# Performance work log

Hardware: AMD Instinct MI355X
Metric: run time of the kernel (lower is better)

The kernel has to match this reference:

```python
import jax, jax.numpy as jnp
import numpy as np

MODEL_DIM = 256
NUM_HEADS = 4
HEAD_DIM = MODEL_DIM // NUM_HEADS
MAX_LEN = 512
EPS = 1e-5


def positional_embedding(n, dim):
    pos = jnp.arange(n, dtype=jnp.float32)[:, None]
    div = jnp.exp(jnp.arange(0, dim, 2, dtype=jnp.float32) * (-np.log(10000.0) / dim))
    pe = jnp.zeros((n, dim), dtype=jnp.float32)
    pe = pe.at[:, 0::2].set(jnp.sin(pos * div))
    pe = pe.at[:, 1::2].set(jnp.cos(pos * div))
    return pe


def layer_norm(x, g, b):
    mu = jnp.mean(x, axis=-1, keepdims=True)
    var = jnp.mean(jnp.square(x - mu), axis=-1, keepdims=True)
    return (x - mu) * jax.lax.rsqrt(var + EPS) * g + b


def setup_inputs() -> dict:
    key = jax.random.key(0)
    ks = jax.random.split(key, 20)
    B, N = 64, 512
    d = MODEL_DIM

    def lin(k, fan_in, fan_out):
        lim = 1.0 / np.sqrt(fan_in)
        return jax.random.uniform(k, (fan_out, fan_in), jnp.float32, -lim, lim)

    def xavier(k, fan_in, fan_out):
        lim = np.sqrt(6.0 / (fan_in + fan_out))
        return jax.random.uniform(k, (fan_out, fan_in), jnp.float32, -lim, lim)

    return {
        "x": jax.random.normal(ks[0], (B, N, 769), jnp.float32),
        "y": jax.random.normal(ks[1], (B, N, 674), jnp.float32),
        "z": jnp.zeros((B, 1), jnp.float32),
        "Wr": lin(ks[2], 769, d), "br": jnp.zeros((d,), jnp.float32),
        "Wf": lin(ks[3], 674, d), "bf": jnp.zeros((d,), jnp.float32),
        "g_x": jnp.ones((d,), jnp.float32), "b_x": jnp.zeros((d,), jnp.float32),
        "g_y": jnp.ones((d,), jnp.float32), "b_y": jnp.zeros((d,), jnp.float32),
        "Wq": xavier(ks[4], d, d), "bq": jnp.zeros((d,), jnp.float32),
        "Wk": xavier(ks[5], d, d), "bk": jnp.zeros((d,), jnp.float32),
        "Wv": xavier(ks[6], d, d), "bv": jnp.zeros((d,), jnp.float32),
        "Wo": xavier(ks[7], d, d), "bo": jnp.zeros((d,), jnp.float32),
        "g_m": jnp.ones((d,), jnp.float32), "b_m": jnp.zeros((d,), jnp.float32),
        "W1": lin(ks[8], d, d), "b1": jnp.zeros((d,), jnp.float32),
        "W2": lin(ks[9], d, d), "b2": jnp.zeros((d,), jnp.float32),
        "Wc": lin(ks[10], d, 2), "bc": jnp.zeros((2,), jnp.float32),
    }


def reference(x, y, z, Wr, br, Wf, bf, g_x, b_x, g_y, b_y,
              Wq, bq, Wk, bk, Wv, bv, Wo, bo, g_m, b_m,
              W1, b1, W2, b2, Wc, bc):
    B, N, _ = x.shape
    d, H, hd = MODEL_DIM, NUM_HEADS, HEAD_DIM
    pe = positional_embedding(MAX_LEN, d)[:N]  # (N, d)

    xp = layer_norm(x @ Wr.T + br + pe[None], g_x, b_x)  # (B,N,d)
    yp = layer_norm(y @ Wf.T + bf + pe[None], g_y, b_y)

    # cross-attention (non-causal, no masks, eval-mode dropout)
    q = (xp @ Wq.T + bq).reshape(B, N, H, hd)
    k = (yp @ Wk.T + bk).reshape(B, N, H, hd)
    v = (yp @ Wv.T + bv).reshape(B, N, H, hd)
    scale = hd ** -0.5
    scores = jnp.einsum("bshd,bthd->bhst", q, k) * scale  # (B,H,N,N)
    attn = jax.nn.softmax(scores, axis=-1)
    ctx = jnp.einsum("bhst,bthd->bshd", attn, v).reshape(B, N, d)
    attn_out = ctx @ Wo.T + bo

    x_res = layer_norm(xp + attn_out, g_m, b_m)
    mlp = jax.nn.relu(x_res @ W1.T + b1) @ W2.T + b2
    x_mlp = x_res + mlp
    pooled = jnp.mean(x_mlp, axis=1)  # (B,d)
    logits = pooled @ Wc.T + bc  # (B,2)
    return logits
```

## Files before the change

### kernel.cpp

```cpp
#include <hip/hip_runtime.h>
#include <hip/hip_bf16.h>

#define B_   64
#define N_   512
#define D_   256
#define H_   4
#define HD_  64

typedef __hip_bfloat16 bf16;
typedef __attribute__((ext_vector_type(8))) short short8;
typedef __attribute__((ext_vector_type(4))) float floatx4;

__device__ __forceinline__ float bf2f(bf16 v) { return __bfloat162float(v); }
__device__ __forceinline__ unsigned short f2us(float f) {
    bf16 h = __float2bfloat16(f);
    union { bf16 h; unsigned short u; } c; c.h = h; return c.u;
}

typedef __attribute__((address_space(1))) const unsigned int asg_u32;
typedef __attribute__((address_space(3))) unsigned int asl_u32;
__device__ __forceinline__ void gl_lds16(const void* g, void* l) {
    __builtin_amdgcn_global_load_lds((asg_u32*)g, (asl_u32*)l, 16, 0, 0);
}

__global__ __launch_bounds__(256)
void convw_k(const float* __restrict__ Wr, const float* __restrict__ Wf,
             const float* __restrict__ Wq, const float* __restrict__ Wk,
             const float* __restrict__ Wv, const float* __restrict__ Wo,
             const float* __restrict__ W1, const float* __restrict__ W2,
             bf16* __restrict__ dst)
{
    const int seg = blockIdx.y;
    const float* src; int Kreal, Kp; size_t off;
    switch (seg) {
        case 0: src = Wr; Kreal = 769; Kp = 800; off = 0; break;
        case 1: src = Wf; Kreal = 674; Kp = 704; off = 256 * 800; break;
        default:
            src = (seg == 2) ? Wq : (seg == 3) ? Wk : (seg == 4) ? Wv
                : (seg == 5) ? Wo : (seg == 6) ? W1 : W2;
            Kreal = 256; Kp = 256;
            off = 256 * 800 + 256 * 704 + (size_t)(seg - 2) * 256 * 256;
            break;
    }
    const int idx = blockIdx.x * 256 + threadIdx.x;
    if (idx >= 256 * Kp / 8) return;
    const int rowk = idx * 8;
    const int n = rowk / Kp, k0 = rowk % Kp;
    unsigned short tmp[8];
    #pragma unroll
    for (int j = 0; j < 8; ++j) {
        int kk = k0 + j;
        tmp[j] = f2us(kk < Kreal ? src[(size_t)n * Kreal + kk] : 0.f);
    }
    *(short8*)&dst[off + (size_t)rowk] = *(short8*)tmp;
}

__global__ __launch_bounds__(256)
void convx_k(const float* __restrict__ src, bf16* __restrict__ dst,
             int Kreal, int Kp)
{
    const int row = blockIdx.x;
    const float* s = src + (size_t)row * Kreal;
    bf16* d = dst + (size_t)row * Kp;
    for (int c = threadIdx.x; c < Kp; c += 256)
        d[c] = __float2bfloat16(c < Kreal ? s[c] : 0.f);
}

__global__ __launch_bounds__(256)
void pe_k(float* __restrict__ pe)
{
    const int n = blockIdx.x, c = threadIdx.x;
    const int j = c & ~1;
    float freq = __expf(-(float)j * (9.210340371976184f / 256.0f));
    float ang = (float)n * freq;
    pe[n * 256 + c] = (c & 1) ? cosf(ang) : sinf(ang);
}

__global__ __launch_bounds__(256)
void gemm_rp(const bf16* __restrict__ A, int lda,
             const bf16* __restrict__ W, int ldw,
             const float* __restrict__ bias, const bf16* __restrict__ res,
             const float* __restrict__ pe,
             const float* __restrict__ g, const float* __restrict__ bln,
             bf16* __restrict__ C, int Kp, int relu)
{
    __shared__ bf16 As[2][4 * 64 * 8];
    __shared__ bf16 Bs[2][4 * 256 * 8];
    __shared__ float s_mu[64][4], s_sq[64][4];

    const int tid = threadIdx.x;
    const int m0 = blockIdx.x * 64;
    const int lane = tid & 63, w = tid >> 6;
    const int fr = lane & 15, quad = lane >> 4;

    const unsigned short* Ap = (const unsigned short*)A + (size_t)(m0 + lane) * lda + w * 8;
    const unsigned short* Wp = (const unsigned short*)W + (size_t)lane * ldw + w * 8;

    floatx4 acc[4][4] = {};

    gl_lds16(Ap, &As[0][(w * 64 + lane) * 8]);
    #pragma unroll
    for (int i = 0; i < 4; ++i)
        gl_lds16(Wp + (size_t)(i * 64) * ldw, &Bs[0][(w * 256 + i * 64 + lane) * 8]);

    int cur = 0;
    for (int k0 = 0; k0 < Kp; k0 += 32) {
        __syncthreads();
        if (k0 + 32 < Kp) {
            const int nb = cur ^ 1;
            gl_lds16(Ap + k0 + 32, &As[nb][(w * 64 + lane) * 8]);
            #pragma unroll
            for (int i = 0; i < 4; ++i)
                gl_lds16(Wp + (size_t)(i * 64) * ldw + k0 + 32,
                         &Bs[nb][(w * 256 + i * 64 + lane) * 8]);
        }
        short8 a[4];
        #pragma unroll
        for (int im = 0; im < 4; ++im)
            a[im] = *(const short8*)&As[cur][(quad * 64 + im * 16 + fr) * 8];
        #pragma unroll
        for (int in = 0; in < 4; ++in) {
            short8 bfrag = *(const short8*)&Bs[cur][(quad * 256 + w * 64 + in * 16 + fr) * 8];
            #pragma unroll
            for (int im = 0; im < 4; ++im)
                acc[im][in] = __builtin_amdgcn_mfma_f32_16x16x32_bf16(
                    a[im], bfrag, acc[im][in], 0, 0, 0);
        }
        cur ^= 1;
    }

    #pragma unroll
    for (int in = 0; in < 4; ++in) {
        const int n = w * 64 + in * 16 + fr;
        const float bi = bias[n];
        #pragma unroll
        for (int im = 0; im < 4; ++im) {
            #pragma unroll
            for (int reg = 0; reg < 4; ++reg) {
                const int m = m0 + im * 16 + quad * 4 + reg;
                float v = acc[im][in][reg] + bi;
                if (pe)   v += pe[((m & (N_ - 1)) << 8) + n];
                if (relu) v = fmaxf(v, 0.f);
                if (res)  v += bf2f(res[((size_t)m << 8) + n]);
                acc[im][in][reg] = v;
            }
        }
    }

    if (g) {
        #pragma unroll
        for (int im = 0; im < 4; ++im) {
            #pragma unroll
            for (int reg = 0; reg < 4; ++reg) {
                float ps = acc[im][0][reg] + acc[im][1][reg]
                         + acc[im][2][reg] + acc[im][3][reg];
                float pq = acc[im][0][reg] * acc[im][0][reg]
                         + acc[im][1][reg] * acc[im][1][reg]
                         + acc[im][2][reg] * acc[im][2][reg]
                         + acc[im][3][reg] * acc[im][3][reg];
                #pragma unroll
                for (int off = 1; off < 16; off <<= 1) {
                    ps += __shfl_xor(ps, off, 64);
                    pq += __shfl_xor(pq, off, 64);
                }
                if (fr == 0) {
                    const int r = im * 16 + quad * 4 + reg;
                    s_mu[r][w] = ps;
                    s_sq[r][w] = pq;
                }
            }
        }
        __syncthreads();
        #pragma unroll
        for (int im = 0; im < 4; ++im) {
            #pragma unroll
            for (int reg = 0; reg < 4; ++reg) {
                const int r = im * 16 + quad * 4 + reg;
                const float mu = (s_mu[r][0] + s_mu[r][1] + s_mu[r][2] + s_mu[r][3])
                                 * (1.f / 256.f);
                const float var = (s_sq[r][0] + s_sq[r][1] + s_sq[r][2] + s_sq[r][3])
                                  * (1.f / 256.f) - mu * mu;
                const float rs = rsqrtf(var + 1e-5f);
                const int m = m0 + r;
                #pragma unroll
                for (int in = 0; in < 4; ++in) {
                    const int n = w * 64 + in * 16 + fr;
                    C[((size_t)m << 8) + n] = __float2bfloat16(
                        (acc[im][in][reg] - mu) * rs * g[n] + bln[n]);
                }
            }
        }
    } else {
        #pragma unroll
        for (int im = 0; im < 4; ++im) {
            #pragma unroll
            for (int reg = 0; reg < 4; ++reg) {
                const int m = m0 + im * 16 + quad * 4 + reg;
                #pragma unroll
                for (int in = 0; in < 4; ++in) {
                    const int n = w * 64 + in * 16 + fr;
                    C[((size_t)m << 8) + n] = __float2bfloat16(acc[im][in][reg]);
                }
            }
        }
    }
}

__global__ __launch_bounds__(256)
void attn_k(const bf16* q, const bf16* __restrict__ k,
            const bf16* __restrict__ v, bf16* ctx)
{
    __shared__ bf16 Qs[8 * 64 * 8];
    __shared__ bf16 Ks[8 * 64 * 8];
    __shared__ bf16 Vs[8 * 64 * 8];
    __shared__ bf16 Ps[4 * 16 * 72];

    const int tid = threadIdx.x;
    const int qt = blockIdx.x & 7;
    const int h  = (blockIdx.x >> 3) & 3;
    const int b  = blockIdx.x >> 5;
    const int q0 = qt * 64;
    const size_t base = ((size_t)b * N_) * D_ + h * HD_;

    const int lane = tid & 63;
    const int w = tid >> 6;
    const int fr = lane & 15, quad = lane >> 4;

    {
        const int row = tid >> 2, c = tid & 3;
        const unsigned short* src = (const unsigned short*)q + base + (size_t)(q0 + row) * D_ + c * 16;
        *(short8*)&Qs[((c * 2 + 0) * 64 + row) * 8] = *(const short8*)(src);
        *(short8*)&Qs[((c * 2 + 1) * 64 + row) * 8] = *(const short8*)(src + 8);
    }
    __syncthreads();

    short8 aq[2];
    #pragma unroll
    for (int ks = 0; ks < 2; ++ks)
        aq[ks] = *(const short8*)&Qs[((ks * 4 + quad) * 64 + w * 16 + fr) * 8];

    floatx4 O[4] = {};
    float mrun[4], lrun[4];
    #pragma unroll
    for (int r = 0; r < 4; ++r) { mrun[r] = -1e30f; lrun[r] = 0.f; }

    for (int kt = 0; kt < 8; ++kt) {
        __syncthreads();
        {
            const int row = tid >> 2, c = tid & 3;
            const unsigned short* srck = (const unsigned short*)k + base + (size_t)(kt * 64 + row) * D_ + c * 16;
            *(short8*)&Ks[((c * 2 + 0) * 64 + row) * 8] = *(const short8*)(srck);
            *(short8*)&Ks[((c * 2 + 1) * 64 + row) * 8] = *(const short8*)(srck + 8);

            const int key = row, gk = key >> 3, jk = key & 7;
            const unsigned short* srcv = (const unsigned short*)v + base + (size_t)(kt * 64 + key) * D_ + c * 16;
            #pragma unroll
            for (int u = 0; u < 4; ++u) {
                ushort4 vv = *(const ushort4*)(srcv + u * 4);
                const int d0 = c * 16 + u * 4;
                Vs[(gk * 64 + d0 + 0) * 8 + jk] = *(bf16*)&vv.x;
                Vs[(gk * 64 + d0 + 1) * 8 + jk] = *(bf16*)&vv.y;
                Vs[(gk * 64 + d0 + 2) * 8 + jk] = *(bf16*)&vv.z;
                Vs[(gk * 64 + d0 + 3) * 8 + jk] = *(bf16*)&vv.w;
            }
        }
        __syncthreads();

        floatx4 S[4] = {};
        #pragma unroll
        for (int in = 0; in < 4; ++in) {
            #pragma unroll
            for (int ks = 0; ks < 2; ++ks) {
                short8 bk = *(const short8*)&Ks[((ks * 4 + quad) * 64 + in * 16 + fr) * 8];
                S[in] = __builtin_amdgcn_mfma_f32_16x16x32_bf16(aq[ks], bk, S[in], 0, 0, 0);
            }
        }
        #pragma unroll
        for (int in = 0; in < 4; ++in) S[in] *= 0.125f;

        #pragma unroll
        for (int r = 0; r < 4; ++r) {
            float mloc = fmaxf(fmaxf(S[0][r], S[1][r]), fmaxf(S[2][r], S[3][r]));
            #pragma unroll
            for (int off = 1; off < 16; off <<= 1) mloc = fmaxf(mloc, __shfl_xor(mloc, off, 64));
            float mnew = fmaxf(mrun[r], mloc);
            float alpha = __expf(mrun[r] - mnew);
            float rs = 0.f;
            #pragma unroll
            for (int in = 0; in < 4; ++in) {
                float p = __expf(S[in][r] - mnew);
                S[in][r] = p;
                rs += p;
            }
            #pragma unroll
            for (int off = 1; off < 16; off <<= 1) rs += __shfl_xor(rs, off, 64);
            lrun[r] = lrun[r] * alpha + rs;
            mrun[r] = mnew;
            #pragma unroll
            for (int in = 0; in < 4; ++in) O[in][r] *= alpha;
        }

        #pragma unroll
        for (int in = 0; in < 4; ++in)
            #pragma unroll
            for (int r = 0; r < 4; ++r)
                Ps[(w * 16 + quad * 4 + r) * 72 + in * 16 + fr] = __float2bfloat16(S[in][r]);
        short8 pa[2];
        #pragma unroll
        for (int ks = 0; ks < 2; ++ks)
            pa[ks] = *(const short8*)&Ps[(w * 16 + fr) * 72 + ks * 32 + quad * 8];

        #pragma unroll
        for (int in = 0; in < 4; ++in) {
            #pragma unroll
            for (int ks = 0; ks < 2; ++ks) {
                short8 bv = *(const short8*)&Vs[((ks * 4 + quad) * 64 + in * 16 + fr) * 8];
                O[in] = __builtin_amdgcn_mfma_f32_16x16x32_bf16(pa[ks], bv, O[in], 0, 0, 0);
            }
        }
    }

    #pragma unroll
    for (int r = 0; r < 4; ++r) {
        const float inv = 1.f / lrun[r];
        const int row = q0 + w * 16 + quad * 4 + r;
        #pragma unroll
        for (int in = 0; in < 4; ++in)
            ctx[base + (size_t)row * D_ + in * 16 + fr] = __float2bfloat16(O[in][r] * inv);
    }
}

__global__ __launch_bounds__(256)
void pool_k(const bf16* __restrict__ x, float* __restrict__ partial)
{
    int b = blockIdx.x, ch = blockIdx.y, c = threadIdx.x;
    float s = 0.f;
    for (int n = ch * 64; n < ch * 64 + 64; ++n)
        s += bf2f(x[((size_t)b * N_ + n) * D_ + c]);
    partial[((size_t)b * 8 + ch) * D_ + c] = s;
}

__global__ __launch_bounds__(256)
void logits_k(const float* __restrict__ partial, const float* __restrict__ Wc,
              const float* __restrict__ bc, float* __restrict__ out)
{
    __shared__ float pl[256];
    __shared__ float red[256];
    int b = blockIdx.x, c = threadIdx.x;
    float s = 0.f;
    for (int ch = 0; ch < 8; ++ch) s += partial[((size_t)b * 8 + ch) * D_ + c];
    pl[c] = s * (1.f / 512.f);
    __syncthreads();
    int o = c >> 7, cc = c & 127;
    red[c] = pl[cc] * Wc[o * 256 + cc] + pl[cc + 128] * Wc[o * 256 + cc + 128];
    __syncthreads();
    for (int st = 64; st > 0; st >>= 1) { if (cc < st) red[c] += red[c + st]; __syncthreads(); }
    if (cc == 0) out[b * 2 + o] = red[c] + bc[o];
}

extern "C" void kernel_launch(void* const* d_in, const int* in_sizes, int n_in,
                              void* d_out, int out_size, void* d_ws, size_t ws_size,
                              hipStream_t stream)
{
    const float* x   = (const float*)d_in[0];
    const float* y   = (const float*)d_in[1];
    const float* Wr  = (const float*)d_in[3];
    const float* br  = (const float*)d_in[4];
    const float* Wf  = (const float*)d_in[5];
    const float* bfv = (const float*)d_in[6];
    const float* gx  = (const float*)d_in[7];
    const float* bx  = (const float*)d_in[8];
    const float* gy  = (const float*)d_in[9];
    const float* by  = (const float*)d_in[10];
    const float* Wq  = (const float*)d_in[11];
    const float* bq  = (const float*)d_in[12];
    const float* Wk  = (const float*)d_in[13];
    const float* bk  = (const float*)d_in[14];
    const float* Wv  = (const float*)d_in[15];
    const float* bv  = (const float*)d_in[16];
    const float* Wo  = (const float*)d_in[17];
    const float* bo  = (const float*)d_in[18];
    const float* gm  = (const float*)d_in[19];
    const float* bm  = (const float*)d_in[20];
    const float* W1  = (const float*)d_in[21];
    const float* b1  = (const float*)d_in[22];
    const float* W2  = (const float*)d_in[23];
    const float* b2  = (const float*)d_in[24];
    const float* Wc  = (const float*)d_in[25];
    const float* bc  = (const float*)d_in[26];

    bf16* ws = (bf16*)d_ws;
    const size_t S = (size_t)B_ * N_ * D_;
    bf16*  wb   = ws;
    float* pe   = (float*)(ws + 778240);
    float* part = pe + 131072;
    bf16*  bA   = ws + 778240 + 4 * 131072;
    bf16*  bB   = bA + S;
    bf16*  bC   = bB + S;
    bf16*  bD   = bC + S;
    bf16*  bE   = bD + S;
    bf16*  xyb  = bC;

    bf16* Wrb = wb;
    bf16* Wfb = wb + 256 * 800;
    bf16* Wqb = Wfb + 256 * 704;
    bf16* Wkb = Wqb + 65536;
    bf16* Wvb = Wkb + 65536;
    bf16* Wob = Wvb + 65536;
    bf16* W1b = Wob + 65536;
    bf16* W2b = W1b + 65536;

    const int M = B_ * N_;
    dim3 blk(256);
    dim3 grp(M / 64);

    pe_k<<<N_, blk, 0, stream>>>(pe);
    convw_k<<<dim3(100, 8), blk, 0, stream>>>(Wr, Wf, Wq, Wk, Wv, Wo, W1, W2, wb);

    convx_k<<<M, blk, 0, stream>>>(x, xyb, 769, 800);
    gemm_rp<<<grp, blk, 0, stream>>>(xyb, 800, Wrb, 800, br, nullptr, pe, gx, bx, bA, 800, 0);
    convx_k<<<M, blk, 0, stream>>>(y, xyb, 674, 704);
    gemm_rp<<<grp, blk, 0, stream>>>(xyb, 704, Wfb, 704, bfv, nullptr, pe, gy, by, bB, 704, 0);
    gemm_rp<<<grp, blk, 0, stream>>>(bA, 256, Wqb, 256, bq, nullptr, nullptr, nullptr, nullptr, bC, 256, 0);
    gemm_rp<<<grp, blk, 0, stream>>>(bB, 256, Wkb, 256, bk, nullptr, nullptr, nullptr, nullptr, bD, 256, 0);
    gemm_rp<<<grp, blk, 0, stream>>>(bB, 256, Wvb, 256, bv, nullptr, nullptr, nullptr, nullptr, bE, 256, 0);
    attn_k<<<B_ * H_ * 8, blk, 0, stream>>>(bC, bD, bE, bC);
    gemm_rp<<<grp, blk, 0, stream>>>(bC, 256, Wob, 256, bo, bA, nullptr, gm, bm, bD, 256, 0);
    gemm_rp<<<grp, blk, 0, stream>>>(bD, 256, W1b, 256, b1, nullptr, nullptr, nullptr, nullptr, bE, 256, 1);
    gemm_rp<<<grp, blk, 0, stream>>>(bE, 256, W2b, 256, b2, bD, nullptr, nullptr, nullptr, bB, 256, 0);
    pool_k<<<dim3(B_, 8), blk, 0, stream>>>(bB, part);
    logits_k<<<B_, blk, 0, stream>>>(part, Wc, bc, (float*)d_out);
}
```

Measured before the change: 613.1 us.

## Fuse input conversion, pooling and V transpose into GEMMs; tune attention softmax

The first two projection GEMMs now read the fp32 inputs directly and convert to bf16 in registers while staging into LDS. This removes the separate convert kernels and their bf16 round trip through global memory. The V projection writes its output pre-transposed, so attention loads K and V with plain vector copies, and Q fragments come straight from global memory. Attention also gains a block-index swizzle, an exp2 softmax with the scale folded in, and MFMA priority hints. Mean pooling is folded into the W2 GEMM epilogue as per-tile column sums. The cost is that the A operand in the fp32 path uses synchronous, unaligned scalar loads with an extra barrier per K step.

```diff
diff --git a/kernel.cpp b/kernel.cpp
--- a/kernel.cpp
+++ b/kernel.cpp
@@ -56,17 +56,6 @@
 }
 
 __global__ __launch_bounds__(256)
-void convx_k(const float* __restrict__ src, bf16* __restrict__ dst,
-             int Kreal, int Kp)
-{
-    const int row = blockIdx.x;
-    const float* s = src + (size_t)row * Kreal;
-    bf16* d = dst + (size_t)row * Kp;
-    for (int c = threadIdx.x; c < Kp; c += 256)
-        d[c] = __float2bfloat16(c < Kreal ? s[c] : 0.f);
-}
-
-__global__ __launch_bounds__(256)
 void pe_k(float* __restrict__ pe)
 {
     const int n = blockIdx.x, c = threadIdx.x;
@@ -76,13 +65,16 @@
     pe[n * 256 + c] = (c & 1) ? cosf(ang) : sinf(ang);
 }
 
+template<bool F32A>
 __global__ __launch_bounds__(256)
-void gemm_rp(const bf16* __restrict__ A, int lda,
-             const bf16* __restrict__ W, int ldw,
-             const float* __restrict__ bias, const bf16* __restrict__ res,
-             const float* __restrict__ pe,
-             const float* __restrict__ g, const float* __restrict__ bln,
-             bf16* __restrict__ C, int Kp, int relu)
+void gemm_rp_t(const bf16* __restrict__ A, const float* __restrict__ A32,
+               int lda, int Kreal,
+               const bf16* __restrict__ W, int ldw,
+               const float* __restrict__ bias, const bf16* __restrict__ res,
+               const float* __restrict__ pe,
+               const float* __restrict__ g, const float* __restrict__ bln,
+               bf16* __restrict__ C, float* __restrict__ pp,
+               int Kp, int relu, int tv)
 {
     __shared__ bf16 As[2][4 * 64 * 8];
     __shared__ bf16 Bs[2][4 * 256 * 8];
@@ -93,40 +85,88 @@
     const int lane = tid & 63, w = tid >> 6;
     const int fr = lane & 15, quad = lane >> 4;
 
-    const unsigned short* Ap = (const unsigned short*)A + (size_t)(m0 + lane) * lda + w * 8;
     const unsigned short* Wp = (const unsigned short*)W + (size_t)lane * ldw + w * 8;
 
     floatx4 acc[4][4] = {};
-
-    gl_lds16(Ap, &As[0][(w * 64 + lane) * 8]);
-    #pragma unroll
-    for (int i = 0; i < 4; ++i)
-        gl_lds16(Wp + (size_t)(i * 64) * ldw, &Bs[0][(w * 256 + i * 64 + lane) * 8]);
-
     int cur = 0;
-    for (int k0 = 0; k0 < Kp; k0 += 32) {
-        __syncthreads();
-        if (k0 + 32 < Kp) {
-            const int nb = cur ^ 1;
-            gl_lds16(Ap + k0 + 32, &As[nb][(w * 64 + lane) * 8]);
-            #pragma unroll
-            for (int i = 0; i < 4; ++i)
-                gl_lds16(Wp + (size_t)(i * 64) * ldw + k0 + 32,
-                         &Bs[nb][(w * 256 + i * 64 + lane) * 8]);
-        }
-        short8 a[4];
-        #pragma unroll
-        for (int im = 0; im < 4; ++im)
-            a[im] = *(const short8*)&As[cur][(quad * 64 + im * 16 + fr) * 8];
-        #pragma unroll
-        for (int in = 0; in < 4; ++in) {
-            short8 bfrag = *(const short8*)&Bs[cur][(quad * 256 + w * 64 + in * 16 + fr) * 8];
+
+    if constexpr (F32A) {
+        const int srow = tid >> 2, skb = tid & 3;
+        const float* a32p = A32 + (size_t)(m0 + srow) * Kreal + skb * 8;
+        float av[8];
+        #pragma unroll
+        for (int j = 0; j < 8; ++j) {
+            int kk = skb * 8 + j;
+            av[j] = (kk < Kreal) ? a32p[j] : 0.f;
+        }
+        #pragma unroll
+        for (int i = 0; i < 4; ++i)
+            gl_lds16(Wp + (size_t)(i * 64) * ldw, &Bs[0][(w * 256 + i * 64 + lane) * 8]);
+
+        for (int k0 = 0; k0 < Kp; k0 += 32) {
+            __syncthreads();
+            unsigned short uw[8];
+            #pragma unroll
+            for (int j = 0; j < 8; ++j) uw[j] = f2us(av[j]);
+            *(short8*)&As[0][(skb * 64 + srow) * 8] = *(short8*)uw;
+            __syncthreads();
+            if (k0 + 32 < Kp) {
+                const int nb = cur ^ 1;
+                #pragma unroll
+                for (int i = 0; i < 4; ++i)
+                    gl_lds16(Wp + (size_t)(i * 64) * ldw + k0 + 32,
+                             &Bs[nb][(w * 256 + i * 64 + lane) * 8]);
+                #pragma unroll
+                for (int j = 0; j < 8; ++j) {
+                    int kk = k0 + 32 + skb * 8 + j;
+                    av[j] = (kk < Kreal) ? a32p[k0 + 32 + j] : 0.f;
+                }
+            }
+            short8 a[4];
             #pragma unroll
             for (int im = 0; im < 4; ++im)
-                acc[im][in] = __builtin_amdgcn_mfma_f32_16x16x32_bf16(
-                    a[im], bfrag, acc[im][in], 0, 0, 0);
-        }
-        cur ^= 1;
+                a[im] = *(const short8*)&As[0][(quad * 64 + im * 16 + fr) * 8];
+            #pragma unroll
+            for (int in = 0; in < 4; ++in) {
+                short8 bfrag = *(const short8*)&Bs[cur][(quad * 256 + w * 64 + in * 16 + fr) * 8];
+                #pragma unroll
+                for (int im = 0; im < 4; ++im)
+                    acc[im][in] = __builtin_amdgcn_mfma_f32_16x16x32_bf16(
+                        a[im], bfrag, acc[im][in], 0, 0, 0);
+            }
+            cur ^= 1;
+        }
+    } else {
+        const unsigned short* Ap = (const unsigned short*)A + (size_t)(m0 + lane) * lda + w * 8;
+        gl_lds16(Ap, &As[0][(w * 64 + lane) * 8]);
+        #pragma unroll
+        for (int i = 0; i < 4; ++i)
+            gl_lds16(Wp + (size_t)(i * 64) * ldw, &Bs[0][(w * 256 + i * 64 + lane) * 8]);
+
+        for (int k0 = 0; k0 < Kp; k0 += 32) {
+            __syncthreads();
+            if (k0 + 32 < Kp) {
+                const int nb = cur ^ 1;
+                gl_lds16(Ap + k0 + 32, &As[nb][(w * 64 + lane) * 8]);
+                #pragma unroll
+                for (int i = 0; i < 4; ++i)
+                    gl_lds16(Wp + (size_t)(i * 64) * ldw + k0 + 32,
+                             &Bs[nb][(w * 256 + i * 64 + lane) * 8]);
+            }
+            short8 a[4];
+            #pragma unroll
+            for (int im = 0; im < 4; ++im)
+                a[im] = *(const short8*)&As[cur][(quad * 64 + im * 16 + fr) * 8];
+            #pragma unroll
+            for (int in = 0; in < 4; ++in) {
+                short8 bfrag = *(const short8*)&Bs[cur][(quad * 256 + w * 64 + in * 16 + fr) * 8];
+                #pragma unroll
+                for (int im = 0; im < 4; ++im)
+                    acc[im][in] = __builtin_amdgcn_mfma_f32_16x16x32_bf16(
+                        a[im], bfrag, acc[im][in], 0, 0, 0);
+            }
+            cur ^= 1;
+        }
     }
 
     #pragma unroll
@@ -190,6 +230,22 @@
                 }
             }
         }
+    } else if (tv) {
+        const int bh = ((m0 >> 9) << 2) + w;
+        const int nn = m0 & (N_ - 1);
+        unsigned short* Ct = (unsigned short*)C;
+        #pragma unroll
+        for (int in = 0; in < 4; ++in) {
+            const int d = in * 16 + fr;
+            #pragma unroll
+            for (int im = 0; im < 4; ++im) {
+                unsigned short pk[4];
+                #pragma unroll
+                for (int reg = 0; reg < 4; ++reg) pk[reg] = f2us(acc[im][in][reg]);
+                *(ushort4*)&Ct[((size_t)(bh * 64 + d) << 9) + nn + im * 16 + quad * 4]
+                    = *(ushort4*)pk;
+            }
+        }
     } else {
         #pragma unroll
         for (int im = 0; im < 4; ++im) {
@@ -203,70 +259,75 @@
                 }
             }
         }
+        if (pp) {
+            #pragma unroll
+            for (int in = 0; in < 4; ++in) {
+                float s = 0.f;
+                #pragma unroll
+                for (int im = 0; im < 4; ++im)
+                    #pragma unroll
+                    for (int reg = 0; reg < 4; ++reg) s += acc[im][in][reg];
+                s += __shfl_xor(s, 16, 64);
+                s += __shfl_xor(s, 32, 64);
+                if (quad == 0)
+                    pp[((m0 >> 6) << 8) + w * 64 + in * 16 + fr] = s;
+            }
+        }
     }
 }
 
 __global__ __launch_bounds__(256)
 void attn_k(const bf16* q, const bf16* __restrict__ k,
-            const bf16* __restrict__ v, bf16* ctx)
-{
-    __shared__ bf16 Qs[8 * 64 * 8];
+            const bf16* __restrict__ vt, bf16* ctx)
+{
     __shared__ bf16 Ks[8 * 64 * 8];
     __shared__ bf16 Vs[8 * 64 * 8];
     __shared__ bf16 Ps[4 * 16 * 72];
 
+    const int bid = blockIdx.x;
+    const int l = (bid & 7) * 256 + (bid >> 3);
+    const int qt = l & 7;
+    const int h  = (l >> 3) & 3;
+    const int b  = l >> 5;
+    const int q0 = qt * 64;
+    const size_t base  = ((size_t)b * N_) * D_ + h * HD_;
+    const size_t vbase = ((size_t)(b * H_ + h) * HD_) * N_;
+
     const int tid = threadIdx.x;
-    const int qt = blockIdx.x & 7;
-    const int h  = (blockIdx.x >> 3) & 3;
-    const int b  = blockIdx.x >> 5;
-    const int q0 = qt * 64;
-    const size_t base = ((size_t)b * N_) * D_ + h * HD_;
-
     const int lane = tid & 63;
     const int w = tid >> 6;
     const int fr = lane & 15, quad = lane >> 4;
 
-    {
-        const int row = tid >> 2, c = tid & 3;
-        const unsigned short* src = (const unsigned short*)q + base + (size_t)(q0 + row) * D_ + c * 16;
-        *(short8*)&Qs[((c * 2 + 0) * 64 + row) * 8] = *(const short8*)(src);
-        *(short8*)&Qs[((c * 2 + 1) * 64 + row) * 8] = *(const short8*)(src + 8);
-    }
-    __syncthreads();
-
     short8 aq[2];
     #pragma unroll
     for (int ks = 0; ks < 2; ++ks)
-        aq[ks] = *(const short8*)&Qs[((ks * 4 + quad) * 64 + w * 16 + fr) * 8];
+        aq[ks] = *(const short8*)((const unsigned short*)q + base
+                   + (size_t)(q0 + w * 16 + fr) * D_ + (ks * 4 + quad) * 8);
 
     floatx4 O[4] = {};
     float mrun[4], lrun[4];
     #pragma unroll
     for (int r = 0; r < 4; ++r) { mrun[r] = -1e30f; lrun[r] = 0.f; }
 
+    const int srow = tid >> 2, sc = tid & 3;
+    const unsigned short* kp = (const unsigned short*)k + base + (size_t)srow * D_ + sc * 16;
+    const unsigned short* vp = (const unsigned short*)vt + vbase + (size_t)srow * N_ + sc * 16;
+    const float C1 = 0.125f * 1.44269504f;
+
     for (int kt = 0; kt < 8; ++kt) {
         __syncthreads();
         {
-            const int row = tid >> 2, c = tid & 3;
-            const unsigned short* srck = (const unsigned short*)k + base + (size_t)(kt * 64 + row) * D_ + c * 16;
-            *(short8*)&Ks[((c * 2 + 0) * 64 + row) * 8] = *(const short8*)(srck);
-            *(short8*)&Ks[((c * 2 + 1) * 64 + row) * 8] = *(const short8*)(srck + 8);
-
-            const int key = row, gk = key >> 3, jk = key & 7;
-            const unsigned short* srcv = (const unsigned short*)v + base + (size_t)(kt * 64 + key) * D_ + c * 16;
-            #pragma unroll
-            for (int u = 0; u < 4; ++u) {
-                ushort4 vv = *(const ushort4*)(srcv + u * 4);
-                const int d0 = c * 16 + u * 4;
-                Vs[(gk * 64 + d0 + 0) * 8 + jk] = *(bf16*)&vv.x;
-                Vs[(gk * 64 + d0 + 1) * 8 + jk] = *(bf16*)&vv.y;
-                Vs[(gk * 64 + d0 + 2) * 8 + jk] = *(bf16*)&vv.z;
-                Vs[(gk * 64 + d0 + 3) * 8 + jk] = *(bf16*)&vv.w;
-            }
+            const unsigned short* srck = kp + (size_t)(kt * 64) * D_;
+            *(short8*)&Ks[((sc * 2 + 0) * 64 + srow) * 8] = *(const short8*)(srck);
+            *(short8*)&Ks[((sc * 2 + 1) * 64 + srow) * 8] = *(const short8*)(srck + 8);
+            const unsigned short* srcv = vp + kt * 64;
+            *(short8*)&Vs[((sc * 2 + 0) * 64 + srow) * 8] = *(const short8*)(srcv);
+            *(short8*)&Vs[((sc * 2 + 1) * 64 + srow) * 8] = *(const short8*)(srcv + 8);
         }
         __syncthreads();
 
         floatx4 S[4] = {};
+        __builtin_amdgcn_s_setprio(1);
         #pragma unroll
         for (int in = 0; in < 4; ++in) {
             #pragma unroll
@@ -275,8 +336,7 @@
                 S[in] = __builtin_amdgcn_mfma_f32_16x16x32_bf16(aq[ks], bk, S[in], 0, 0, 0);
             }
         }
-        #pragma unroll
-        for (int in = 0; in < 4; ++in) S[in] *= 0.125f;
+        __builtin_amdgcn_s_setprio(0);
 
         #pragma unroll
         for (int r = 0; r < 4; ++r) {
@@ -284,11 +344,12 @@
             #pragma unroll
             for (int off = 1; off < 16; off <<= 1) mloc = fmaxf(mloc, __shfl_xor(mloc, off, 64));
             float mnew = fmaxf(mrun[r], mloc);
-            float alpha = __expf(mrun[r] - mnew);
+            float mc = mnew * C1;
+            float alpha = exp2f(mrun[r] * C1 - mc);
             float rs = 0.f;
             #pragma unroll
             for (int in = 0; in < 4; ++in) {
-                float p = __expf(S[in][r] - mnew);
+                float p = exp2f(S[in][r] * C1 - mc);
                 S[in][r] = p;
                 rs += p;
             }
@@ -310,6 +371,7 @@
         for (int ks = 0; ks < 2; ++ks)
             pa[ks] = *(const short8*)&Ps[(w * 16 + fr) * 72 + ks * 32 + quad * 8];
 
+        __builtin_amdgcn_s_setprio(1);
         #pragma unroll
         for (int in = 0; in < 4; ++in) {
             #pragma unroll
@@ -318,6 +380,7 @@
                 O[in] = __builtin_amdgcn_mfma_f32_16x16x32_bf16(pa[ks], bv, O[in], 0, 0, 0);
             }
         }
+        __builtin_amdgcn_s_setprio(0);
     }
 
     #pragma unroll
@@ -328,16 +391,6 @@
         for (int in = 0; in < 4; ++in)
             ctx[base + (size_t)row * D_ + in * 16 + fr] = __float2bfloat16(O[in][r] * inv);
     }
-}
-
-__global__ __launch_bounds__(256)
-void pool_k(const bf16* __restrict__ x, float* __restrict__ partial)
-{
-    int b = blockIdx.x, ch = blockIdx.y, c = threadIdx.x;
-    float s = 0.f;
-    for (int n = ch * 64; n < ch * 64 + 64; ++n)
-        s += bf2f(x[((size_t)b * N_ + n) * D_ + c]);
-    partial[((size_t)b * 8 + ch) * D_ + c] = s;
 }
 
 __global__ __launch_bounds__(256)
@@ -399,7 +452,6 @@
     bf16*  bC   = bB + S;
     bf16*  bD   = bC + S;
     bf16*  bE   = bD + S;
-    bf16*  xyb  = bC;
 
     bf16* Wrb = wb;
     bf16* Wfb = wb + 256 * 800;
@@ -417,17 +469,22 @@
     pe_k<<<N_, blk, 0, stream>>>(pe);
     convw_k<<<dim3(100, 8), blk, 0, stream>>>(Wr, Wf, Wq, Wk, Wv, Wo, W1, W2, wb);
 
-    convx_k<<<M, blk, 0, stream>>>(x, xyb, 769, 800);
-    gemm_rp<<<grp, blk, 0, stream>>>(xyb, 800, Wrb, 800, br, nullptr, pe, gx, bx, bA, 800, 0);
-    convx_k<<<M, blk, 0, stream>>>(y, xyb, 674, 704);
-    gemm_rp<<<grp, blk, 0, stream>>>(xyb, 704, Wfb, 704, bfv, nullptr, pe, gy, by, bB, 704, 0);
-    gemm_rp<<<grp, blk, 0, stream>>>(bA, 256, Wqb, 256, bq, nullptr, nullptr, nullptr, nullptr, bC, 256, 0);
-    gemm_rp<<<grp, blk, 0, stream>>>(bB, 256, Wkb, 256, bk, nullptr, nullptr, nullptr, nullptr, bD, 256, 0);
-    gemm_rp<<<grp, blk, 0, stream>>>(bB, 256, Wvb, 256, bv, nullptr, nullptr, nullptr, nullptr, bE, 256, 0);
+    gemm_rp_t<true><<<grp, blk, 0, stream>>>(nullptr, x, 0, 769, Wrb, 800,
+        br, nullptr, pe, gx, bx, bA, nullptr, 800, 0, 0);
+    gemm_rp_t<true><<<grp, blk, 0, stream>>>(nullptr, y, 0, 674, Wfb, 704,
+        bfv, nullptr, pe, gy, by, bB, nullptr, 704, 0, 0);
+    gemm_rp_t<false><<<grp, blk, 0, stream>>>(bA, nullptr, 256, 256, Wqb, 256,
+        bq, nullptr, nullptr, nullptr, nullptr, bC, nullptr, 256, 0, 0);
+    gemm_rp_t<false><<<grp, blk, 0, stream>>>(bB, nullptr, 256, 256, Wkb, 256,
+        bk, nullptr, nullptr, nullptr, nullptr, bD, nullptr, 256, 0, 0);
+    gemm_rp_t<false><<<grp, blk, 0, stream>>>(bB, nullptr, 256, 256, Wvb, 256,
+        bv, nullptr, nullptr, nullptr, nullptr, bE, nullptr, 256, 0, 1);
     attn_k<<<B_ * H_ * 8, blk, 0, stream>>>(bC, bD, bE, bC);
-    gemm_rp<<<grp, blk, 0, stream>>>(bC, 256, Wob, 256, bo, bA, nullptr, gm, bm, bD, 256, 0);
-    gemm_rp<<<grp, blk, 0, stream>>>(bD, 256, W1b, 256, b1, nullptr, nullptr, nullptr, nullptr, bE, 256, 1);
-    gemm_rp<<<grp, blk, 0, stream>>>(bE, 256, W2b, 256, b2, bD, nullptr, nullptr, nullptr, bB, 256, 0);
-    pool_k<<<dim3(B_, 8), blk, 0, stream>>>(bB, part);
+    gemm_rp_t<false><<<grp, blk, 0, stream>>>(bC, nullptr, 256, 256, Wob, 256,
+        bo, bA, nullptr, gm, bm, bD, nullptr, 256, 0, 0);
+    gemm_rp_t<false><<<grp, blk, 0, stream>>>(bD, nullptr, 256, 256, W1b, 256,
+        b1, nullptr, nullptr, nullptr, nullptr, bE, nullptr, 256, 1, 0);
+    gemm_rp_t<false><<<grp, blk, 0, stream>>>(bE, nullptr, 256, 256, W2b, 256,
+        b2, bD, nullptr, nullptr, nullptr, bB, part, 256, 0, 0);
     logits_k<<<B_, blk, 0, stream>>>(part, Wc, bc, (float*)d_out);
 }
```

Result: faster. 569.7 us (-7.1%).
